# Performance work log

Measured on AMD Instinct MI355X. Metric: run time of the kernel, lower is better.

The kernel has to match this reference:

```python
import jax, jax.numpy as jnp
import numpy as np

SMALL_NUMBER = 1e-7
N_NODES = 100000
FEAT = 512
N_GRAPHS = 512


def setup_inputs() -> dict:
    key = jax.random.key(0)
    k1, k2 = jax.random.split(key)
    node_features = jax.random.normal(k1, (N_NODES, FEAT), dtype=jnp.float32)
    node_to_graph_map = jnp.sort(
        jax.random.randint(k2, (N_NODES,), 0, N_GRAPHS, dtype=jnp.int32)
    )
    alpha = jnp.ones((FEAT,), dtype=jnp.float32)
    beta = jnp.zeros((FEAT,), dtype=jnp.float32)
    gamma = jnp.ones((FEAT,), dtype=jnp.float32)
    return {
        "node_features": node_features,
        "node_to_graph_map": node_to_graph_map,
        "alpha": alpha,
        "beta": beta,
        "gamma": gamma,
        "num_segments": N_GRAPHS,
    }


def _segment_mean(data, segment_ids, num_segments):
    # data: [N, D]; segment_ids: [N] sorted ints in [0, num_segments)
    sums = jax.ops.segment_sum(data, segment_ids, num_segments=num_segments)
    counts = jax.ops.segment_sum(
        jnp.ones((data.shape[0], 1), dtype=data.dtype),
        segment_ids,
        num_segments=num_segments,
    )
    return sums / jnp.maximum(counts, 1.0)


def reference(node_features, node_to_graph_map, alpha, beta, gamma, num_segments):
    # GraphNorm: gamma * (h - alpha*mu) / sigma + beta, per-graph statistics.
    graph_means = _segment_mean(node_features, node_to_graph_map, num_segments)  # [G, D]
    per_node_means = graph_means[node_to_graph_map]  # [N, D]
    centered = node_features - alpha * per_node_means
    graph_vars = _segment_mean(jnp.square(centered), node_to_graph_map, num_segments)  # [G, D]
    per_node_std = jnp.sqrt(graph_vars)[node_to_graph_map]  # [N, D]
    out = centered / (per_node_std + SMALL_NUMBER)
    out = out * gamma + beta
    return out
```

## Files before the change

### kernel.cpp

```cpp
#include <hip/hip_runtime.h>

#define FEAT 512
#define FEAT4 128
#define NGRAPH 512
#define EPS 1e-7f
#define NB 2048
#define MAXSLOT 8

typedef float f32x4 __attribute__((ext_vector_type(4)));

__device__ __forceinline__ int lower_bound(const int* __restrict__ a, int n, int key) {
    int lo = 0, hi = n;
    while (lo < hi) { int mid = (lo + hi) >> 1; if (a[mid] < key) lo = mid + 1; else hi = mid; }
    return lo;
}

__global__ __launch_bounds__(256) void gn_partial(
    const float* __restrict__ feat,
    const int*   __restrict__ map,
    float* __restrict__ PPART,
    int n_nodes, int rpb)
{
    const int b  = blockIdx.x;
    const int rs = b * rpb;
    if (rs >= n_nodes) return;
    const int re = min(rs + rpb, n_nodes);

    const int tid = threadIdx.x;
    const int q = tid & (FEAT4 - 1);
    const int r = tid >> 7;

    const float4* __restrict__ f4 = (const float4*)feat;
    __shared__ float4 lsum[2][FEAT4];
    __shared__ float4 lssq[2][FEAT4];

    int cur = rs;
    int slot;
    {
        const int g0 = map[rs];
        const int gstart0 = lower_bound(map, n_nodes, g0);
        slot = b - gstart0 / rpb;
    }

    while (cur < re) {
        const int g = map[cur];
        int lo = cur + 1, hi = re;
        while (lo < hi) { int mid = (lo + hi) >> 1; if (map[mid] <= g) lo = mid + 1; else hi = mid; }
        const int send = lo;

        float4 sum = make_float4(0.f, 0.f, 0.f, 0.f);
        float4 ssq = make_float4(0.f, 0.f, 0.f, 0.f);
        for (int row = cur + r; row < send; row += 2) {
            float4 v = f4[(size_t)row * FEAT4 + q];
            sum.x += v.x;       sum.y += v.y;       sum.z += v.z;       sum.w += v.w;
            ssq.x += v.x * v.x; ssq.y += v.y * v.y; ssq.z += v.z * v.z; ssq.w += v.w * v.w;
        }
        lsum[r][q] = sum;
        lssq[r][q] = ssq;
        __syncthreads();
        if (r == 0 && slot >= 0 && slot < MAXSLOT) {
            float4 a = lsum[1][q], c = lssq[1][q];
            sum.x += a.x; sum.y += a.y; sum.z += a.z; sum.w += a.w;
            ssq.x += c.x; ssq.y += c.y; ssq.z += c.z; ssq.w += c.w;
            const size_t o = ((size_t)(g * MAXSLOT + slot) * 2) * FEAT4 + q;
            ((float4*)PPART)[o]         = sum;
            ((float4*)PPART)[o + FEAT4] = ssq;
        }
        __syncthreads();
        cur = send;
        slot = 0;
    }
}

__global__ __launch_bounds__(256) void gn_apply(
    const float* __restrict__ feat,
    const int*   __restrict__ map,
    const float* __restrict__ PPART,
    const float* __restrict__ alpha,
    const float* __restrict__ beta,
    const float* __restrict__ gamma,
    float* __restrict__ out,
    int n_nodes, int rpb)
{
    const int b  = blockIdx.x;
    const int rs = b * rpb;
    if (rs >= n_nodes) return;
    const int re = min(rs + rpb, n_nodes);

    const int tid = threadIdx.x;
    const int q = tid & (FEAT4 - 1);
    const int r = tid >> 7;

    const float4* __restrict__ f4 = (const float4*)feat;
    const float4* __restrict__ P4 = (const float4*)PPART;
    f32x4* __restrict__ o4 = (f32x4*)out;

    const float4 al = ((const float4*)alpha)[q];
    const float4 be = ((const float4*)beta)[q];
    const float4 ga = ((const float4*)gamma)[q];

    int cur = rs;
    while (cur < re) {
        const int g = map[cur];
        const int gstart = lower_bound(map, n_nodes, g);
        const int gend   = lower_bound(map, n_nodes, g + 1);
        const int send   = min(gend, re);
        const int cnt    = gend - gstart;
        const int bfirst = gstart / rpb;
        int nslots = (gend - 1) / rpb - bfirst + 1;
        if (nslots > MAXSLOT) nslots = MAXSLOT;

        float4 sum = make_float4(0.f, 0.f, 0.f, 0.f);
        float4 ssq = make_float4(0.f, 0.f, 0.f, 0.f);
        for (int s = 0; s < nslots; ++s) {
            const size_t o = ((size_t)(g * MAXSLOT + s) * 2) * FEAT4 + q;
            float4 a = P4[o], c = P4[o + FEAT4];
            sum.x += a.x; sum.y += a.y; sum.z += a.z; sum.w += a.w;
            ssq.x += c.x; ssq.y += c.y; ssq.z += c.z; ssq.w += c.w;
        }

        const float inv = 1.0f / (float)max(cnt, 1);
        float sv[4], tv[4];
        {
            const float mu[4]  = { sum.x * inv, sum.y * inv, sum.z * inv, sum.w * inv };
            const float msq[4] = { ssq.x * inv, ssq.y * inv, ssq.z * inv, ssq.w * inv };
            const float aa[4]  = { al.x, al.y, al.z, al.w };
            const float bb[4]  = { be.x, be.y, be.z, be.w };
            const float gg[4]  = { ga.x, ga.y, ga.z, ga.w };
            #pragma unroll
            for (int j = 0; j < 4; ++j) {
                float var = msq[j] - mu[j] * mu[j] * (2.0f * aa[j] - aa[j] * aa[j]);
                var = fmaxf(var, 0.0f);
                const float s = gg[j] / (sqrtf(var) + EPS);
                sv[j] = s;
                tv[j] = bb[j] - aa[j] * mu[j] * s;
            }
        }

        for (int row = cur + r; row < send; row += 2) {
            float4 v = f4[(size_t)row * FEAT4 + q];
            f32x4 o;
            o.x = v.x * sv[0] + tv[0];
            o.y = v.y * sv[1] + tv[1];
            o.z = v.z * sv[2] + tv[2];
            o.w = v.w * sv[3] + tv[3];
            __builtin_nontemporal_store(o, &o4[(size_t)row * FEAT4 + q]);
        }
        cur = send;
    }
}

__global__ __launch_bounds__(512) void graphnorm_stats(
    const float* __restrict__ feat,
    const int*   __restrict__ map,
    const float* __restrict__ alpha,
    const float* __restrict__ beta,
    const float* __restrict__ gamma,
    float* __restrict__ S,
    float* __restrict__ T,
    int n_nodes)
{
    const int g = blockIdx.x;
    int lo = 0, hi = n_nodes;
    while (lo < hi) { int mid = (lo + hi) >> 1; if (map[mid] < g) lo = mid + 1; else hi = mid; }
    const int seg_start = lo;
    hi = n_nodes;
    while (lo < hi) { int mid = (lo + hi) >> 1; if (map[mid] < g + 1) lo = mid + 1; else hi = mid; }
    const int seg_end = lo;
    const int cnt = seg_end - seg_start;

    const int tid = threadIdx.x;
    const int q = tid & (FEAT4 - 1);
    const int r = tid >> 7;

    float4 sum = make_float4(0.f, 0.f, 0.f, 0.f);
    float4 ssq = make_float4(0.f, 0.f, 0.f, 0.f);
    const float4* __restrict__ f4 = (const float4*)feat;

    for (int row = seg_start + r; row < seg_end; row += 4) {
        float4 v = f4[(size_t)row * FEAT4 + q];
        sum.x += v.x;       sum.y += v.y;       sum.z += v.z;       sum.w += v.w;
        ssq.x += v.x * v.x; ssq.y += v.y * v.y; ssq.z += v.z * v.z; ssq.w += v.w * v.w;
    }

    __shared__ float4 lsum[4][FEAT4];
    __shared__ float4 lssq[4][FEAT4];
    lsum[r][q] = sum;
    lssq[r][q] = ssq;
    __syncthreads();

    if (r == 0) {
        #pragma unroll
        for (int k = 1; k < 4; ++k) {
            float4 a = lsum[k][q], c = lssq[k][q];
            sum.x += a.x; sum.y += a.y; sum.z += a.z; sum.w += a.w;
            ssq.x += c.x; ssq.y += c.y; ssq.z += c.z; ssq.w += c.w;
        }
        const float inv = 1.0f / (float)max(cnt, 1);
        float4 al = ((const float4*)alpha)[q];
        float4 be = ((const float4*)beta)[q];
        float4 ga = ((const float4*)gamma)[q];
        float mu[4]  = { sum.x * inv, sum.y * inv, sum.z * inv, sum.w * inv };
        float msq[4] = { ssq.x * inv, ssq.y * inv, ssq.z * inv, ssq.w * inv };
        float a[4]   = { al.x, al.y, al.z, al.w };
        float bb[4]  = { be.x, be.y, be.z, be.w };
        float gg[4]  = { ga.x, ga.y, ga.z, ga.w };
        float so[4], to[4];
        #pragma unroll
        for (int j = 0; j < 4; ++j) {
            float var = msq[j] - mu[j] * mu[j] * (2.0f * a[j] - a[j] * a[j]);
            var = fmaxf(var, 0.0f);
            float s = gg[j] / (sqrtf(var) + EPS);
            so[j] = s;
            to[j] = bb[j] - a[j] * mu[j] * s;
        }
        ((float4*)S)[(size_t)g * FEAT4 + q] = make_float4(so[0], so[1], so[2], so[3]);
        ((float4*)T)[(size_t)g * FEAT4 + q] = make_float4(to[0], to[1], to[2], to[3]);
    }
}

__global__ __launch_bounds__(256) void graphnorm_apply_tab(
    const float* __restrict__ feat,
    const int*   __restrict__ map,
    const float* __restrict__ S,
    const float* __restrict__ T,
    float* __restrict__ out,
    long total4)
{
    const float4* __restrict__ f4 = (const float4*)feat;
    const float4* __restrict__ S4 = (const float4*)S;
    const float4* __restrict__ T4 = (const float4*)T;
    f32x4* __restrict__ o4 = (f32x4*)out;

    const long stride = (long)gridDim.x * blockDim.x;
    for (long idx = (long)blockIdx.x * blockDim.x + threadIdx.x; idx < total4; idx += stride) {
        const int n = (int)(idx >> 7);
        const int q = (int)(idx & (FEAT4 - 1));
        const int g = map[n];
        float4 v = f4[idx];
        float4 s = S4[(size_t)g * FEAT4 + q];
        float4 t = T4[(size_t)g * FEAT4 + q];
        f32x4 o;
        o.x = v.x * s.x + t.x;
        o.y = v.y * s.y + t.y;
        o.z = v.z * s.z + t.z;
        o.w = v.w * s.w + t.w;
        __builtin_nontemporal_store(o, &o4[idx]);
    }
}

extern "C" void kernel_launch(void* const* d_in, const int* in_sizes, int n_in,
                              void* d_out, int out_size, void* d_ws, size_t ws_size,
                              hipStream_t stream) {
    const float* feat  = (const float*)d_in[0];
    const int*   map   = (const int*)d_in[1];
    const float* alpha = (const float*)d_in[2];
    const float* beta  = (const float*)d_in[3];
    const float* gamma = (const float*)d_in[4];

    const int n_nodes = in_sizes[1];
    const int rpb = (n_nodes + NB - 1) / NB;

    const size_t ppartBytes = (size_t)NGRAPH * MAXSLOT * 2 * FEAT * sizeof(float);

    if (ws_size >= ppartBytes) {
        float* PPART = (float*)d_ws;
        gn_partial<<<NB, 256, 0, stream>>>(feat, map, PPART, n_nodes, rpb);
        gn_apply<<<NB, 256, 0, stream>>>(feat, map, PPART, alpha, beta, gamma,
                                         (float*)d_out, n_nodes, rpb);
    } else {
        float* S = (float*)d_ws;
        float* T = S + (size_t)NGRAPH * FEAT;
        graphnorm_stats<<<NGRAPH, 512, 0, stream>>>(feat, map, alpha, beta, gamma, S, T, n_nodes);
        const long total4 = (long)n_nodes * FEAT4;
        graphnorm_apply_tab<<<2048, 256, 0, stream>>>(feat, map, S, T, (float*)d_out, total4);
    }
}
```

Before: 113.3 us.

## Precompute segment boundaries, remap block order, and use nontemporal loads in apply

Adds a small kernel that builds a segment-start table from the sorted map, so the partial and apply kernels read segment bounds directly instead of binary-searching the map. Both kernels also remap physical block ids to logical row ranges in a strided pattern, unroll their row loops, and the apply kernel switches to nontemporal vector loads with vector FMA. This removes repeated binary searches and may improve memory-channel spread, at the cost of one extra kernel launch. The fallback path also drops its nontemporal store.

```diff
diff --git a/kernel.cpp b/kernel.cpp
--- a/kernel.cpp
+++ b/kernel.cpp
@@ -3,26 +3,46 @@
 #define FEAT 512
 #define FEAT4 128
 #define NGRAPH 512
-#define EPS 1e-7f
 #define NB 2048
 #define MAXSLOT 8
+#define EPS 1e-7f
 
 typedef float f32x4 __attribute__((ext_vector_type(4)));
 
-__device__ __forceinline__ int lower_bound(const int* __restrict__ a, int n, int key) {
-    int lo = 0, hi = n;
-    while (lo < hi) { int mid = (lo + hi) >> 1; if (a[mid] < key) lo = mid + 1; else hi = mid; }
-    return lo;
+__device__ __forceinline__ void acc4(float4& s, const float4 v) {
+    s.x += v.x; s.y += v.y; s.z += v.z; s.w += v.w;
+}
+__device__ __forceinline__ void accsq4(float4& s, const float4 v) {
+    s.x += v.x * v.x; s.y += v.y * v.y; s.z += v.z * v.z; s.w += v.w * v.w;
+}
+__device__ __forceinline__ float4 add4(const float4 a, const float4 b) {
+    return make_float4(a.x + b.x, a.y + b.y, a.z + b.z, a.w + b.w);
+}
+__device__ __forceinline__ int logical_block(int pb, int nb) {
+    return (pb & 7) * (nb >> 3) + (pb >> 3);
+}
+
+__global__ __launch_bounds__(256) void gn_bounds(
+    const int* __restrict__ map, int* __restrict__ segstart, int n_nodes)
+{
+    const int i = blockIdx.x * blockDim.x + threadIdx.x;
+    if (i >= n_nodes) return;
+    const int cur  = map[i];
+    const int prev = (i == 0) ? -1 : map[i - 1];
+    for (int g = prev + 1; g <= cur; ++g) segstart[g] = i;
+    if (i == n_nodes - 1)
+        for (int g = cur + 1; g <= NGRAPH; ++g) segstart[g] = n_nodes;
 }
 
 __global__ __launch_bounds__(256) void gn_partial(
     const float* __restrict__ feat,
     const int*   __restrict__ map,
-    float* __restrict__ PPART,
+    const int*   __restrict__ segstart,
+    float*       __restrict__ PPART,
     int n_nodes, int rpb)
 {
-    const int b  = blockIdx.x;
-    const int rs = b * rpb;
+    const int lb = logical_block(blockIdx.x, gridDim.x);
+    const int rs = lb * rpb;
     if (rs >= n_nodes) return;
     const int re = min(rs + rpb, n_nodes);
 
@@ -30,44 +50,36 @@
     const int q = tid & (FEAT4 - 1);
     const int r = tid >> 7;
 
-    const float4* __restrict__ f4 = (const float4*)feat;
     __shared__ float4 lsum[2][FEAT4];
     __shared__ float4 lssq[2][FEAT4];
+    const float4* __restrict__ f4 = (const float4*)feat;
+    float4* __restrict__ P4 = (float4*)PPART;
 
     int cur = rs;
-    int slot;
-    {
-        const int g0 = map[rs];
-        const int gstart0 = lower_bound(map, n_nodes, g0);
-        slot = b - gstart0 / rpb;
-    }
-
+    int g = map[rs];
+    int slot = lb - segstart[g] / rpb;
     while (cur < re) {
-        const int g = map[cur];
-        int lo = cur + 1, hi = re;
-        while (lo < hi) { int mid = (lo + hi) >> 1; if (map[mid] <= g) lo = mid + 1; else hi = mid; }
-        const int send = lo;
+        const int send = min(segstart[g + 1], re);
 
         float4 sum = make_float4(0.f, 0.f, 0.f, 0.f);
         float4 ssq = make_float4(0.f, 0.f, 0.f, 0.f);
+        #pragma unroll 4
         for (int row = cur + r; row < send; row += 2) {
             float4 v = f4[(size_t)row * FEAT4 + q];
-            sum.x += v.x;       sum.y += v.y;       sum.z += v.z;       sum.w += v.w;
-            ssq.x += v.x * v.x; ssq.y += v.y * v.y; ssq.z += v.z * v.z; ssq.w += v.w * v.w;
+            acc4(sum, v);
+            accsq4(ssq, v);
         }
         lsum[r][q] = sum;
         lssq[r][q] = ssq;
         __syncthreads();
         if (r == 0 && slot >= 0 && slot < MAXSLOT) {
-            float4 a = lsum[1][q], c = lssq[1][q];
-            sum.x += a.x; sum.y += a.y; sum.z += a.z; sum.w += a.w;
-            ssq.x += c.x; ssq.y += c.y; ssq.z += c.z; ssq.w += c.w;
             const size_t o = ((size_t)(g * MAXSLOT + slot) * 2) * FEAT4 + q;
-            ((float4*)PPART)[o]         = sum;
-            ((float4*)PPART)[o + FEAT4] = ssq;
+            P4[o]         = add4(lsum[0][q], lsum[1][q]);
+            P4[o + FEAT4] = add4(lssq[0][q], lssq[1][q]);
         }
         __syncthreads();
         cur = send;
+        if (cur < re) g = map[cur];
         slot = 0;
     }
 }
@@ -75,15 +87,16 @@
 __global__ __launch_bounds__(256) void gn_apply(
     const float* __restrict__ feat,
     const int*   __restrict__ map,
+    const int*   __restrict__ segstart,
     const float* __restrict__ PPART,
     const float* __restrict__ alpha,
     const float* __restrict__ beta,
     const float* __restrict__ gamma,
-    float* __restrict__ out,
+    float*       __restrict__ out,
     int n_nodes, int rpb)
 {
-    const int b  = blockIdx.x;
-    const int rs = b * rpb;
+    const int lb = logical_block(blockIdx.x, gridDim.x);
+    const int rs = lb * rpb;
     if (rs >= n_nodes) return;
     const int re = min(rs + rpb, n_nodes);
 
@@ -91,7 +104,7 @@
     const int q = tid & (FEAT4 - 1);
     const int r = tid >> 7;
 
-    const float4* __restrict__ f4 = (const float4*)feat;
+    const f32x4* __restrict__ f4n = (const f32x4*)feat;
     const float4* __restrict__ P4 = (const float4*)PPART;
     f32x4* __restrict__ o4 = (f32x4*)out;
 
@@ -100,10 +113,10 @@
     const float4 ga = ((const float4*)gamma)[q];
 
     int cur = rs;
+    int g = map[rs];
     while (cur < re) {
-        const int g = map[cur];
-        const int gstart = lower_bound(map, n_nodes, g);
-        const int gend   = lower_bound(map, n_nodes, g + 1);
+        const int gstart = segstart[g];
+        const int gend   = segstart[g + 1];
         const int send   = min(gend, re);
         const int cnt    = gend - gstart;
         const int bfirst = gstart / rpb;
@@ -114,13 +127,12 @@
         float4 ssq = make_float4(0.f, 0.f, 0.f, 0.f);
         for (int s = 0; s < nslots; ++s) {
             const size_t o = ((size_t)(g * MAXSLOT + s) * 2) * FEAT4 + q;
-            float4 a = P4[o], c = P4[o + FEAT4];
-            sum.x += a.x; sum.y += a.y; sum.z += a.z; sum.w += a.w;
-            ssq.x += c.x; ssq.y += c.y; ssq.z += c.z; ssq.w += c.w;
+            acc4(sum, P4[o]);
+            acc4(ssq, P4[o + FEAT4]);
         }
 
         const float inv = 1.0f / (float)max(cnt, 1);
-        float sv[4], tv[4];
+        f32x4 sv, tv;
         {
             const float mu[4]  = { sum.x * inv, sum.y * inv, sum.z * inv, sum.w * inv };
             const float msq[4] = { ssq.x * inv, ssq.y * inv, ssq.z * inv, ssq.w * inv };
@@ -137,16 +149,15 @@
             }
         }
 
+        #pragma unroll 4
         for (int row = cur + r; row < send; row += 2) {
-            float4 v = f4[(size_t)row * FEAT4 + q];
-            f32x4 o;
-            o.x = v.x * sv[0] + tv[0];
-            o.y = v.y * sv[1] + tv[1];
-            o.z = v.z * sv[2] + tv[2];
-            o.w = v.w * sv[3] + tv[3];
-            __builtin_nontemporal_store(o, &o4[(size_t)row * FEAT4 + q]);
+            const size_t idx = (size_t)row * FEAT4 + q;
+            f32x4 v = __builtin_nontemporal_load(&f4n[idx]);
+            f32x4 o = v * sv + tv;
+            __builtin_nontemporal_store(o, &o4[idx]);
         }
         cur = send;
+        if (cur < re) g = map[cur];
     }
 }
 
@@ -179,8 +190,8 @@
 
     for (int row = seg_start + r; row < seg_end; row += 4) {
         float4 v = f4[(size_t)row * FEAT4 + q];
-        sum.x += v.x;       sum.y += v.y;       sum.z += v.z;       sum.w += v.w;
-        ssq.x += v.x * v.x; ssq.y += v.y * v.y; ssq.z += v.z * v.z; ssq.w += v.w * v.w;
+        acc4(sum, v);
+        accsq4(ssq, v);
     }
 
     __shared__ float4 lsum[4][FEAT4];
@@ -192,9 +203,8 @@
     if (r == 0) {
         #pragma unroll
         for (int k = 1; k < 4; ++k) {
-            float4 a = lsum[k][q], c = lssq[k][q];
-            sum.x += a.x; sum.y += a.y; sum.z += a.z; sum.w += a.w;
-            ssq.x += c.x; ssq.y += c.y; ssq.z += c.z; ssq.w += c.w;
+            acc4(sum, lsum[k][q]);
+            acc4(ssq, lssq[k][q]);
         }
         const float inv = 1.0f / (float)max(cnt, 1);
         float4 al = ((const float4*)alpha)[q];
@@ -245,7 +255,7 @@
         o.y = v.y * s.y + t.y;
         o.z = v.z * s.z + t.z;
         o.w = v.w * s.w + t.w;
-        __builtin_nontemporal_store(o, &o4[idx]);
+        o4[idx] = o;
     }
 }
 
@@ -261,12 +271,18 @@
     const int n_nodes = in_sizes[1];
     const int rpb = (n_nodes + NB - 1) / NB;
 
-    const size_t ppartBytes = (size_t)NGRAPH * MAXSLOT * 2 * FEAT * sizeof(float);
-
-    if (ws_size >= ppartBytes) {
-        float* PPART = (float*)d_ws;
-        gn_partial<<<NB, 256, 0, stream>>>(feat, map, PPART, n_nodes, rpb);
-        gn_apply<<<NB, 256, 0, stream>>>(feat, map, PPART, alpha, beta, gamma,
+    const size_t ppartElems = (size_t)NGRAPH * MAXSLOT * 2 * FEAT;
+    const size_t needBytes  = ppartElems * 4 + (NGRAPH + 1) * sizeof(int);
+
+    if (ws_size >= needBytes) {
+        float* PPART   = (float*)d_ws;
+        int*   SEGSTART = (int*)((float*)d_ws + ppartElems);
+
+        const int bblocks = (n_nodes + 255) / 256;
+        gn_bounds<<<bblocks, 256, 0, stream>>>(map, SEGSTART, n_nodes);
+        gn_partial<<<NB, 256, 0, stream>>>(feat, map, SEGSTART, PPART, n_nodes, rpb);
+        gn_apply<<<NB, 256, 0, stream>>>(feat, map, SEGSTART, PPART,
+                                         alpha, beta, gamma,
                                          (float*)d_out, n_nodes, rpb);
     } else {
         float* S = (float*)d_ws;
```

Result: no change. 111.3 us (-1.8%).
